# Kernel tuning notes

Hardware: AMD Instinct MI355X
Metric: run time of the kernel (lower is better)

Reference implementation:

```python
import jax, jax.numpy as jnp
import numpy as np

B, C, FH, FW = 2, 256, 256, 256
N_ROIS = 512
OUT_SIZE = 7
MAX_POOL = True
GRID = OUT_SIZE * (2 if MAX_POOL else 1)  # 14: internal sampling grid
SPATIAL_SCALE = 0.0625  # 1/16 -> image is 4096x4096


def setup_inputs() -> dict:
    key = jax.random.key(0)
    k1, k2, k3, k4, k5 = jax.random.split(key, 5)
    features = jax.random.normal(k1, (B, C, FH, FW), dtype=jnp.float32)
    img = FW / SPATIAL_SCALE  # 4096
    idx = jax.random.randint(k2, (N_ROIS,), 0, B).astype(jnp.float32)
    cx = jax.random.uniform(k3, (N_ROIS, 2), minval=0.125 * img, maxval=0.875 * img)
    wh = jax.random.uniform(k4, (N_ROIS, 2), minval=64.0, maxval=1024.0)
    theta = jax.random.uniform(k5, (N_ROIS,), minval=-np.pi / 2, maxval=np.pi / 2)
    x1 = cx[:, 0] - wh[:, 0] / 2; x2 = cx[:, 0] + wh[:, 0] / 2
    y1 = cx[:, 1] - wh[:, 1] / 2; y2 = cx[:, 1] + wh[:, 1] / 2
    rois = jnp.stack([idx, x1, y1, x2, y2, theta], axis=1).astype(jnp.float32)
    return {"features": features, "rois": rois}


def _rotated_roi_pool(features, rois):
    fh, fw = features.shape[-2:]
    idxs = rois[:, 0].astype(jnp.int32)
    x1, y1, x2, y2, th = (rois[:, k] for k in range(1, 6))
    cx, cy = (x1 + x2) * 0.5, (y1 + y2) * 0.5
    w, h = x2 - x1, y2 - y1
    cos_t, sin_t = jnp.cos(th), jnp.sin(th)
    inv_s = 1.0 / SPATIAL_SCALE

    # affine_grid base coords, align_corners=False: pixel centers in [-1,1]
    base = (2.0 * jnp.arange(GRID, dtype=jnp.float32) + 1.0) / GRID - 1.0
    ux = base[None, None, :]  # [1,1,G] (x varies along columns)
    uy = base[None, :, None]  # [1,G,1]

    # inverse of cv2 affine chain: p = c + (1/s) * Rot(-theta) @ diag(w/2,h/2) @ u
    def e(v):
        return v[:, None, None]
    px = e(cx) + inv_s * (e(cos_t * w * 0.5) * ux + e(sin_t * h * 0.5) * uy)
    py = e(cy) + inv_s * (e(-sin_t * w * 0.5) * ux + e(cos_t * h * 0.5) * uy)
    # normalized feature coords, then grid_sample pixel coords (align_corners=False)
    gx = 2.0 * px / fw - 1.0
    gy = 2.0 * py / fh - 1.0
    ix = ((gx + 1.0) * fw - 1.0) * 0.5  # [N,G,G]
    iy = ((gy + 1.0) * fh - 1.0) * 0.5

    ix0 = jnp.floor(ix); iy0 = jnp.floor(iy)
    wx = ix - ix0; wy = iy - iy0
    ix0 = ix0.astype(jnp.int32); iy0 = iy0.astype(jnp.int32)
    ix1 = ix0 + 1; iy1 = iy0 + 1

    imgs = features[idxs]  # [N,C,H,W]
    n = jnp.arange(idxs.shape[0])[:, None, None]

    def gather(yi, xi):
        valid = (yi >= 0) & (yi < fh) & (xi >= 0) & (xi < fw)
        yc = jnp.clip(yi, 0, fh - 1)
        xc = jnp.clip(xi, 0, fw - 1)
        v = imgs[n, :, yc, xc]  # [N,G,G,C]
        return v * valid[..., None].astype(v.dtype)

    out = (gather(iy0, ix0) * ((1 - wy) * (1 - wx))[..., None]
           + gather(iy0, ix1) * ((1 - wy) * wx)[..., None]
           + gather(iy1, ix0) * (wy * (1 - wx))[..., None]
           + gather(iy1, ix1) * (wy * wx)[..., None])  # [N,G,G,C]
    out = jnp.transpose(out, (0, 3, 1, 2))  # [N,C,G,G]

    if MAX_POOL:
        n_, c_ = out.shape[:2]
        out = out.reshape(n_, c_, GRID // 2, 2, GRID // 2, 2).max(axis=(3, 5))
    return out


def reference(features, rois):
    return _rotated_roi_pool(features, rois)
```

## Files before the change

kernel.cpp:

```cpp
#include <hip/hip_runtime.h>

#define NC   256
#define FHH  256
#define FWW  256
#define NOUT 7
#define NCELL 49

__global__ __launch_bounds__(256) void rroi_pool_kernel(
    const float* __restrict__ feat, const float* __restrict__ rois,
    float* __restrict__ out)
{
    const int cell = blockIdx.x;
    const int n    = blockIdx.y;
    const int c    = threadIdx.x;
    const int ph = cell / NOUT;
    const int pw = cell % NOUT;

    const float* r = rois + (size_t)n * 6;
    const int   idx = (int)r[0];
    const float x1 = r[1], y1 = r[2], x2 = r[3], y2 = r[4], th = r[5];
    const float cx = (x1 + x2) * 0.5f;
    const float cy = (y1 + y2) * 0.5f;
    const float w  = x2 - x1;
    const float h  = y2 - y1;
    const float cos_t = cosf(th), sin_t = sinf(th);

    const float awx =  cos_t * w * 0.5f;
    const float bwy =  sin_t * h * 0.5f;
    const float cwx = -sin_t * w * 0.5f;
    const float dwy =  cos_t * h * 0.5f;

    const float* __restrict__ img =
        feat + ((size_t)idx * NC + c) * (size_t)(FHH * FWW);

    float m = -3.402823466e+38f;

#pragma unroll
    for (int dy = 0; dy < 2; ++dy) {
#pragma unroll
        for (int dx = 0; dx < 2; ++dx) {
            const int gy = 2 * ph + dy;
            const int gx = 2 * pw + dx;
            const float uy = (2.0f * (float)gy + 1.0f) / 14.0f - 1.0f;
            const float ux = (2.0f * (float)gx + 1.0f) / 14.0f - 1.0f;

            const float px = cx + 16.0f * (awx * ux + bwy * uy);
            const float py = cy + 16.0f * (cwx * ux + dwy * uy);

            const float gxn = 2.0f * px / 256.0f - 1.0f;
            const float gyn = 2.0f * py / 256.0f - 1.0f;
            const float ixf = ((gxn + 1.0f) * 256.0f - 1.0f) * 0.5f;
            const float iyf = ((gyn + 1.0f) * 256.0f - 1.0f) * 0.5f;

            const float ix0f = floorf(ixf);
            const float iy0f = floorf(iyf);
            const float wx = ixf - ix0f;
            const float wy = iyf - iy0f;
            const int ix0 = (int)ix0f;
            const int iy0 = (int)iy0f;
            const int ix1 = ix0 + 1;
            const int iy1 = iy0 + 1;

            const bool vx0 = (ix0 >= 0) & (ix0 < FWW);
            const bool vx1 = (ix1 >= 0) & (ix1 < FWW);
            const bool vy0 = (iy0 >= 0) & (iy0 < FHH);
            const bool vy1 = (iy1 >= 0) & (iy1 < FHH);

            float val = 0.0f;
            if ((vy0 | vy1) & (vx0 | vx1)) {
                const int xc0 = min(max(ix0, 0), FWW - 1);
                const int xc1 = min(max(ix1, 0), FWW - 1);
                const int yc0 = min(max(iy0, 0), FHH - 1);
                const int yc1 = min(max(iy1, 0), FHH - 1);
                const float v00 = img[yc0 * FWW + xc0] * (float)(vy0 & vx0);
                const float v01 = img[yc0 * FWW + xc1] * (float)(vy0 & vx1);
                const float v10 = img[yc1 * FWW + xc0] * (float)(vy1 & vx0);
                const float v11 = img[yc1 * FWW + xc1] * (float)(vy1 & vx1);
                val = v00 * ((1.0f - wy) * (1.0f - wx))
                    + v01 * ((1.0f - wy) * wx)
                    + v10 * (wy * (1.0f - wx))
                    + v11 * (wy * wx);
            }
            m = fmaxf(m, val);
        }
    }

    out[((size_t)n * NC + c) * NCELL + cell] = m;
}

extern "C" void kernel_launch(void* const* d_in, const int* in_sizes, int n_in,
                              void* d_out, int out_size, void* d_ws, size_t ws_size,
                              hipStream_t stream) {
    const float* feat = (const float*)d_in[0];
    const float* rois = (const float*)d_in[1];
    float* out = (float*)d_out;
    const int nrois = in_sizes[1] / 6;
    dim3 grid(NCELL, nrois);
    rroi_pool_kernel<<<grid, 256, 0, stream>>>(feat, rois, out);
}
```

Before: 212.9 us.

## Process one ROI per block with shared sample table and coalesced output

Launches one block per ROI instead of one per output cell, computing the 196 bilinear sample offsets and weights once into shared memory. Each thread (channel) then loops over all 49 cells, stages results in shared memory, and writes the ROI's output with coalesced float4 stores. This removes redundant coordinate math and strided output writes, but shrinks the grid to one block per ROI and uses about 50KB of shared memory per block, reducing occupancy for a latency-bound gather.

```diff
diff --git a/kernel.cpp b/kernel.cpp
--- a/kernel.cpp
+++ b/kernel.cpp
@@ -1,91 +1,113 @@
 #include <hip/hip_runtime.h>
+#include <float.h>
 
-#define NC   256
-#define FHH  256
-#define FWW  256
-#define NOUT 7
+#define NC    256
+#define FHH   256
+#define FWW   256
+#define NOUT  7
 #define NCELL 49
+#define NSAMP (NCELL * 4)
 
-__global__ __launch_bounds__(256) void rroi_pool_kernel(
+__global__ __launch_bounds__(256) void rroi_pool_roi_kernel(
     const float* __restrict__ feat, const float* __restrict__ rois,
     float* __restrict__ out)
 {
-    const int cell = blockIdx.x;
-    const int n    = blockIdx.y;
-    const int c    = threadIdx.x;
-    const int ph = cell / NOUT;
-    const int pw = cell % NOUT;
+    __shared__ int4   s_off[NSAMP];
+    __shared__ float4 s_wt[NSAMP];
+    __shared__ int    s_any[NSAMP];
+    __shared__ float  s_out[NC * NCELL];
 
-    const float* r = rois + (size_t)n * 6;
-    const int   idx = (int)r[0];
-    const float x1 = r[1], y1 = r[2], x2 = r[3], y2 = r[4], th = r[5];
-    const float cx = (x1 + x2) * 0.5f;
-    const float cy = (y1 + y2) * 0.5f;
-    const float w  = x2 - x1;
-    const float h  = y2 - y1;
-    const float cos_t = cosf(th), sin_t = sinf(th);
+    const int n = blockIdx.x;
+    const int tid = threadIdx.x;
+    const float* __restrict__ r = rois + (size_t)n * 6;
 
-    const float awx =  cos_t * w * 0.5f;
-    const float bwy =  sin_t * h * 0.5f;
-    const float cwx = -sin_t * w * 0.5f;
-    const float dwy =  cos_t * h * 0.5f;
+    if (tid < NSAMP) {
+        const int cell = tid >> 2;
+        const int sub  = tid & 3;
+        const int ph = cell / NOUT, pw = cell % NOUT;
+        const int dy = sub >> 1,    dx = sub & 1;
+        const int gy = 2 * ph + dy;
+        const int gx = 2 * pw + dx;
 
+        const float x1 = r[1], y1 = r[2], x2 = r[3], y2 = r[4], th = r[5];
+        const float cx = (x1 + x2) * 0.5f;
+        const float cy = (y1 + y2) * 0.5f;
+        const float w  = x2 - x1;
+        const float h  = y2 - y1;
+        const float cos_t = cosf(th), sin_t = sinf(th);
+        const float awx =  cos_t * w * 0.5f;
+        const float bwy =  sin_t * h * 0.5f;
+        const float cwx = -sin_t * w * 0.5f;
+        const float dwy =  cos_t * h * 0.5f;
+
+        const float uy = (2.0f * (float)gy + 1.0f) / 14.0f - 1.0f;
+        const float ux = (2.0f * (float)gx + 1.0f) / 14.0f - 1.0f;
+
+        const float px = cx + 16.0f * (awx * ux + bwy * uy);
+        const float py = cy + 16.0f * (cwx * ux + dwy * uy);
+
+        const float gxn = 2.0f * px / 256.0f - 1.0f;
+        const float gyn = 2.0f * py / 256.0f - 1.0f;
+        const float ixf = ((gxn + 1.0f) * 256.0f - 1.0f) * 0.5f;
+        const float iyf = ((gyn + 1.0f) * 256.0f - 1.0f) * 0.5f;
+
+        const float ix0f = floorf(ixf);
+        const float iy0f = floorf(iyf);
+        const float wx = ixf - ix0f;
+        const float wy = iyf - iy0f;
+        const int ix0 = (int)ix0f;
+        const int iy0 = (int)iy0f;
+        const int ix1 = ix0 + 1;
+        const int iy1 = iy0 + 1;
+
+        const bool vx0 = (ix0 >= 0) & (ix0 < FWW);
+        const bool vx1 = (ix1 >= 0) & (ix1 < FWW);
+        const bool vy0 = (iy0 >= 0) & (iy0 < FHH);
+        const bool vy1 = (iy1 >= 0) & (iy1 < FHH);
+
+        const int xc0 = min(max(ix0, 0), FWW - 1);
+        const int xc1 = min(max(ix1, 0), FWW - 1);
+        const int yc0 = min(max(iy0, 0), FHH - 1);
+        const int yc1 = min(max(iy1, 0), FHH - 1);
+
+        s_off[tid] = make_int4(yc0 * FWW + xc0, yc0 * FWW + xc1,
+                               yc1 * FWW + xc0, yc1 * FWW + xc1);
+        s_wt[tid] = make_float4(((1.0f - wy) * (1.0f - wx)) * (float)(vy0 & vx0),
+                                ((1.0f - wy) * wx)          * (float)(vy0 & vx1),
+                                (wy * (1.0f - wx))          * (float)(vy1 & vx0),
+                                (wy * wx)                   * (float)(vy1 & vx1));
+        s_any[tid] = (int)((vy0 | vy1) & (vx0 | vx1));
+    }
+    __syncthreads();
+
+    const int c = tid;
+    const int idx = (int)r[0];
     const float* __restrict__ img =
         feat + ((size_t)idx * NC + c) * (size_t)(FHH * FWW);
 
-    float m = -3.402823466e+38f;
-
+    for (int cell = 0; cell < NCELL; ++cell) {
+        float m = -FLT_MAX;
 #pragma unroll
-    for (int dy = 0; dy < 2; ++dy) {
-#pragma unroll
-        for (int dx = 0; dx < 2; ++dx) {
-            const int gy = 2 * ph + dy;
-            const int gx = 2 * pw + dx;
-            const float uy = (2.0f * (float)gy + 1.0f) / 14.0f - 1.0f;
-            const float ux = (2.0f * (float)gx + 1.0f) / 14.0f - 1.0f;
-
-            const float px = cx + 16.0f * (awx * ux + bwy * uy);
-            const float py = cy + 16.0f * (cwx * ux + dwy * uy);
-
-            const float gxn = 2.0f * px / 256.0f - 1.0f;
-            const float gyn = 2.0f * py / 256.0f - 1.0f;
-            const float ixf = ((gxn + 1.0f) * 256.0f - 1.0f) * 0.5f;
-            const float iyf = ((gyn + 1.0f) * 256.0f - 1.0f) * 0.5f;
-
-            const float ix0f = floorf(ixf);
-            const float iy0f = floorf(iyf);
-            const float wx = ixf - ix0f;
-            const float wy = iyf - iy0f;
-            const int ix0 = (int)ix0f;
-            const int iy0 = (int)iy0f;
-            const int ix1 = ix0 + 1;
-            const int iy1 = iy0 + 1;
-
-            const bool vx0 = (ix0 >= 0) & (ix0 < FWW);
-            const bool vx1 = (ix1 >= 0) & (ix1 < FWW);
-            const bool vy0 = (iy0 >= 0) & (iy0 < FHH);
-            const bool vy1 = (iy1 >= 0) & (iy1 < FHH);
-
+        for (int sub = 0; sub < 4; ++sub) {
+            const int s = cell * 4 + sub;
             float val = 0.0f;
-            if ((vy0 | vy1) & (vx0 | vx1)) {
-                const int xc0 = min(max(ix0, 0), FWW - 1);
-                const int xc1 = min(max(ix1, 0), FWW - 1);
-                const int yc0 = min(max(iy0, 0), FHH - 1);
-                const int yc1 = min(max(iy1, 0), FHH - 1);
-                const float v00 = img[yc0 * FWW + xc0] * (float)(vy0 & vx0);
-                const float v01 = img[yc0 * FWW + xc1] * (float)(vy0 & vx1);
-                const float v10 = img[yc1 * FWW + xc0] * (float)(vy1 & vx0);
-                const float v11 = img[yc1 * FWW + xc1] * (float)(vy1 & vx1);
-                val = v00 * ((1.0f - wy) * (1.0f - wx))
-                    + v01 * ((1.0f - wy) * wx)
-                    + v10 * (wy * (1.0f - wx))
-                    + v11 * (wy * wx);
+            if (s_any[s]) {
+                const int4   o = s_off[s];
+                const float4 wv = s_wt[s];
+                val = img[o.x] * wv.x + img[o.y] * wv.y
+                    + img[o.z] * wv.z + img[o.w] * wv.w;
             }
             m = fmaxf(m, val);
         }
+        s_out[c * NCELL + cell] = m;
     }
+    __syncthreads();
 
-    out[((size_t)n * NC + c) * NCELL + cell] = m;
+    float4* __restrict__ dst = (float4*)(out + (size_t)n * (NC * NCELL));
+    const float4* __restrict__ src = (const float4*)s_out;
+#pragma unroll
+    for (int i = tid; i < (NC * NCELL) / 4; i += 256)
+        dst[i] = src[i];
 }
 
 extern "C" void kernel_launch(void* const* d_in, const int* in_sizes, int n_in,
@@ -95,6 +117,5 @@
     const float* rois = (const float*)d_in[1];
     float* out = (float*)d_out;
     const int nrois = in_sizes[1] / 6;
-    dim3 grid(NCELL, nrois);
-    rroi_pool_kernel<<<grid, 256, 0, stream>>>(feat, rois, out);
+    rroi_pool_roi_kernel<<<nrois, 256, 0, stream>>>(feat, rois, out);
 }
```

Result: faster. 179.6 us (-15.6%).
